# Performance work log

Hardware: AMD Instinct MI355X
Metric: run time of the kernel (lower is better)

The kernel has to match this reference:

```python
import jax, jax.numpy as jnp
import numpy as np

B, Q, K, D = 32, 1024, 1024, 128

def setup_inputs() -> dict:
    key = jax.random.key(0)
    kq, kk, kv, kl = jax.random.split(key, 4)
    return {
        "queries": jax.random.normal(kq, (B, Q, D), dtype=jnp.float32),
        "keys": jax.random.normal(kk, (B, K, D), dtype=jnp.float32),
        "values": jax.random.normal(kv, (B, K, D), dtype=jnp.float32),
        "valid_length": jax.random.randint(kl, (B,), 1, K + 1),
    }

def reference(queries, keys, values, valid_length):
    d = queries.shape[-1]
    # scores: [B, Q, K]
    scores = jnp.einsum("bqd,bkd->bqk", queries, keys) / jnp.sqrt(jnp.float32(d))
    # length mask: position k is valid iff k < valid_length[b]
    mask = jnp.arange(keys.shape[1])[None, None, :] < valid_length[:, None, None]
    scores = jnp.where(mask, scores, jnp.float32(-1e9))
    attn = jax.nn.softmax(scores, axis=-1)
    # dropout module is identity in eval / p=0
    return jnp.einsum("bqk,bkv->bqv", attn, values)
```

## Files before the change

### kernel.cpp

```cpp
#include <hip/hip_runtime.h>
#include <hip/hip_bf16.h>
#include <stdint.h>

#define B_    32
#define QLEN  1024
#define KSEQ  1024
#define DIM   128
#define NKT   (KSEQ / 64)
#define SCALE 0.08838834764831845f
#define KSC   0.12751879522655792f

typedef __attribute__((ext_vector_type(8)))  short short8;
typedef __attribute__((ext_vector_type(4)))  float floatx4;
typedef __attribute__((ext_vector_type(16))) float floatx16;
typedef unsigned int u32;

__device__ __forceinline__ u32 f2bf(float x) {
  union { float f; u32 u; } v; v.f = x;
  return (v.u + 0x7FFF + ((v.u >> 16) & 1)) >> 16;
}
__device__ __forceinline__ u32 pack2(float lo, float hi) {
  return f2bf(lo) | (f2bf(hi) << 16);
}
__device__ __forceinline__ u32 cvtpk(float lo, float hi) {
  u32 d;
  asm("v_cvt_pk_bf16_f32 %0, %1, %2" : "=v"(d) : "v"(lo), "v"(hi));
  return d;
}
__device__ __forceinline__ void swap32(u32& a, u32& b) {
  asm volatile("v_permlane32_swap_b32 %0, %1" : "+v"(a), "+v"(b));
}
__device__ __forceinline__ float exp2_fast(float x) {
  float d;
  asm("v_exp_f32 %0, %1" : "=v"(d) : "v"(x));
  return d;
}
typedef union { uint4 u; short8 s; } U8;

__global__ __launch_bounds__(256) void prep_kernel(const float* __restrict__ Kg,
                                                   const float* __restrict__ Vg,
                                                   const int* __restrict__ vlen,
                                                   uint4* __restrict__ Ksw,
                                                   uint4* __restrict__ Vsw,
                                                   int2* __restrict__ task) {
  __shared__ __align__(16) u32 Vu[64 * 65];
  __shared__ int sidx[32];
  const int kt = blockIdx.x, b = blockIdx.y, t = threadIdx.x;
  const bool tableblk = (blockIdx.z == 0) && (kt == 0) && (b == 0);

  if (tableblk && t < 64) {
    const int bb = t & 31;
    const int ntb = (vlen[bb] + 63) >> 6;
    int rank = 0;
#pragma unroll
    for (int j = 0; j < 32; j++) {
      const int ntj = __shfl(ntb, j);
      rank += (ntj > ntb) | ((ntj == ntb) & (j < bb));
    }
    if (t < 32) sidx[rank] = bb;
  }

  if (kt * 64 < vlen[b]) {
    if (blockIdx.z == 0) {
      const float* src = Kg + ((size_t)b * KSEQ + kt * 64) * DIM;
      uint4* dst = Ksw + ((size_t)b * NKT + kt) * 1024;
#pragma unroll
      for (int it = 0; it < 4; it++) {
        const int f = it * 256 + t, r = f >> 4, c = f & 15;
        floatx4 f0 = *(const floatx4*)(src + r * DIM + c * 8);
        floatx4 f1 = *(const floatx4*)(src + r * DIM + c * 8 + 4);
        uint4 o;
        o.x = pack2(f0[0] * KSC, f0[1] * KSC); o.y = pack2(f0[2] * KSC, f0[3] * KSC);
        o.z = pack2(f1[0] * KSC, f1[1] * KSC); o.w = pack2(f1[2] * KSC, f1[3] * KSC);
        dst[r * 16 + (c ^ (r & 15))] = o;
      }
    } else {
      const float* src = Vg + ((size_t)b * KSEQ + kt * 64) * DIM;
#pragma unroll
      for (int it = 0; it < 8; it++) {
        const int k = it * 8 + (t >> 5), c = t & 31;
        const floatx4 f = *(const floatx4*)(src + (size_t)k * DIM + c * 4);
        const int s = (k >> 3) & 4;
        Vu[k * 65 + ((2 * c) ^ s)]     = pack2(f[0], f[1]);
        Vu[k * 65 + ((2 * c + 1) ^ s)] = pack2(f[2], f[3]);
      }
      __syncthreads();
      uint4* dst = Vsw + ((size_t)b * NKT + kt) * 1024;
#pragma unroll
      for (int it = 0; it < 4; it++) {
        const int id = it * 256 + t;
        const int kc = id & 7, d = (id >> 3) & 127;
        const int col = (d >> 1) ^ (kc & 4);
        u32 r[8];
#pragma unroll
        for (int j = 0; j < 8; j++) r[j] = Vu[(kc * 8 + j) * 65 + col];
        const u32 sel = (d & 1) ? 0x07060302u : 0x05040100u;
        uint4 o;
        o.x = __builtin_amdgcn_perm(r[1], r[0], sel);
        o.y = __builtin_amdgcn_perm(r[3], r[2], sel);
        o.z = __builtin_amdgcn_perm(r[5], r[4], sel);
        o.w = __builtin_amdgcn_perm(r[7], r[6], sel);
        dst[d * 8 + (kc ^ (d & 7))] = o;
      }
    }
  }

  if (tableblk) {
    __syncthreads();
    for (int l = t; l < 512; l += 256) {
      const int x = l & 7, j = l >> 3;
      int rank, q;
      if (j < 32) { rank = (j & 1) ? x + 8  : x;      q = j >> 1; }
      else        { rank = (j & 1) ? x + 16 : x + 24; q = (j - 32) >> 1; }
      task[l] = make_int2(sidx[rank], q << 6);
    }
  }
}

__global__ __launch_bounds__(256, 2) void attn_kernel(
    const float* __restrict__ Qg, const uint4* __restrict__ Ksw,
    const uint4* __restrict__ Vsw, const int* __restrict__ vlen,
    const int2* __restrict__ task, float* __restrict__ Og) {
  __shared__ float scr[64 * 128];
  __shared__ float Lred[2][32];

  const int2 tq = task[blockIdx.x];
  const int b = tq.x, q0 = tq.y;
  const int t = threadIdx.x, wave = t >> 6, lane = t & 63;
  const int qh = wave & 1, kh = wave >> 1;
  const int l31 = lane & 31, hi = lane >> 5, m15 = l31 & 15, m7 = l31 & 7;
  const int L  = vlen[b];
  const int nt = (L + 63) >> 6;
  const int krow = kh * 32 + l31;

  const short* KtS = (const short*)(Ksw + (size_t)b * NKT * 1024);
  const short* Vt  = (const short*)(Vsw + (size_t)b * NKT * 1024);

  short8 qb[8];
  {
    const float* qrow = Qg + ((size_t)b * QLEN + q0 + qh * 32 + l31) * DIM;
#pragma unroll
    for (int c = 0; c < 8; c++) {
      floatx4 f0 = *(const floatx4*)(qrow + c * 16 + hi * 8);
      floatx4 f1 = *(const floatx4*)(qrow + c * 16 + hi * 8 + 4);
      short8 a;
      a[0] = (short)f2bf(f0[0]); a[1] = (short)f2bf(f0[1]);
      a[2] = (short)f2bf(f0[2]); a[3] = (short)f2bf(f0[3]);
      a[4] = (short)f2bf(f1[0]); a[5] = (short)f2bf(f1[1]);
      a[6] = (short)f2bf(f1[2]); a[7] = (short)f2bf(f1[3]);
      qb[c] = a;
    }
  }

  float lrow = 0.0f;
  floatx16 oacc[4];
#pragma unroll
  for (int dt = 0; dt < 4; dt++)
#pragma unroll
    for (int i = 0; i < 16; i++) oacc[dt][i] = 0.0f;

#define LOAD_K(DST, tkv)                                                       \
  {                                                                            \
    const short* kp_ = KtS + (size_t)(tkv) * 8192 + krow * 128;                \
    _Pragma("unroll") for (int c_ = 0; c_ < 8; c_++)                           \
      DST[c_] = *(const short8*)(kp_ + ((2 * c_ + hi) ^ m15) * 8);             \
  }

#define BODY(KF, tkv)                                                          \
  {                                                                            \
    const int k0_ = (tkv) * 64;                                                \
    short8 vb[4][2];                                                           \
    {                                                                          \
      const short* vt_ = Vt + (size_t)(tkv) * 8192;                            \
      _Pragma("unroll") for (int dt = 0; dt < 4; dt++) {                       \
        const short* vr_ = vt_ + (dt * 32 + l31) * 64;                         \
        vb[dt][0] = *(const short8*)(vr_ + ((kh * 4 + 0 + hi) ^ m7) * 8);      \
        vb[dt][1] = *(const short8*)(vr_ + ((kh * 4 + 2 + hi) ^ m7) * 8);      \
      }                                                                        \
    }                                                                          \
    floatx16 s;                                                                \
    _Pragma("unroll") for (int i = 0; i < 16; i++) s[i] = 0.0f;                \
    __builtin_amdgcn_s_setprio(1);                                             \
    _Pragma("unroll") for (int c = 0; c < 8; c++)                              \
      s = __builtin_amdgcn_mfma_f32_32x32x16_bf16(KF[c], qb[c], s, 0, 0, 0);   \
    __builtin_amdgcn_s_setprio(0);                                             \
    if (k0_ + kh * 32 + 32 <= L) {                                             \
      _Pragma("unroll") for (int r = 0; r < 16; r++) {                         \
        s[r] = exp2_fast(s[r]);                                                \
        lrow += s[r];                                                          \
      }                                                                        \
    } else {                                                                   \
      _Pragma("unroll") for (int r = 0; r < 16; r++) {                         \
        const int ck = (r & 3) + 8 * (r >> 2) + 4 * hi;                        \
        const float a = (k0_ + kh * 32 + ck < L) ? exp2_fast(s[r]) : 0.0f;     \
        s[r] = a;                                                              \
        lrow += a;                                                             \
      }                                                                        \
    }                                                                          \
    {                                                                          \
      u32 u0 = cvtpk(s[0], s[1]),   u1 = cvtpk(s[2], s[3]);                    \
      u32 u2 = cvtpk(s[4], s[5]),   u3 = cvtpk(s[6], s[7]);                    \
      swap32(u0, u2); swap32(u1, u3);                                          \
      u32 w0 = cvtpk(s[8], s[9]),   w1 = cvtpk(s[10], s[11]);                  \
      u32 w2 = cvtpk(s[12], s[13]), w3 = cvtpk(s[14], s[15]);                  \
      swap32(w0, w2); swap32(w1, w3);                                          \
      U8 pu0; pu0.u.x = u0; pu0.u.y = u1; pu0.u.z = u2; pu0.u.w = u3;          \
      U8 pu1; pu1.u.x = w0; pu1.u.y = w1; pu1.u.z = w2; pu1.u.w = w3;          \
      __builtin_amdgcn_s_setprio(1);                                           \
      _Pragma("unroll") for (int dt = 0; dt < 4; dt++) {                       \
        oacc[dt] = __builtin_amdgcn_mfma_f32_32x32x16_bf16(pu0.s, vb[dt][0],   \
                                                           oacc[dt], 0, 0, 0);\
        oacc[dt] = __builtin_amdgcn_mfma_f32_32x32x16_bf16(pu1.s, vb[dt][1],   \
                                                           oacc[dt], 0, 0, 0);\
      }                                                                        \
      __builtin_amdgcn_s_setprio(0);                                           \
    }                                                                          \
  }

  short8 ka[8], kb[8];
  LOAD_K(ka, 0);
  int tk = 0;
  for (;;) {
    if (tk + 1 < nt) LOAD_K(kb, tk + 1);
    BODY(ka, tk);
    if (++tk == nt) break;
    if (tk + 1 < nt) LOAD_K(ka, tk + 1);
    BODY(kb, tk);
    if (++tk == nt) break;
  }

  lrow += __shfl_xor(lrow, 32);
  if (kh == 1) {
    if (lane < 32) Lred[qh][l31] = lrow;
#pragma unroll
    for (int dt = 0; dt < 4; dt++)
#pragma unroll
      for (int r = 0; r < 16; r++)
        scr[(dt * 16 + r) * 128 + qh * 64 + lane] = oacc[dt][r];
  }
  __syncthreads();
  if (kh == 0) {
    const float ltot = lrow + Lred[qh][l31];
    const float inv_ = 1.0f / ltot;
    float iv[16];
#pragma unroll
    for (int r = 0; r < 16; r++)
      iv[r] = __shfl(inv_, (r & 3) + 8 * (r >> 2) + 4 * hi);
    float* obase = Og + ((size_t)b * QLEN + q0 + qh * 32) * DIM + l31;
#pragma unroll
    for (int dt = 0; dt < 4; dt++) {
#pragma unroll
      for (int r = 0; r < 16; r++) {
        const int rq = (r & 3) + 8 * (r >> 2) + 4 * hi;
        const float v = oacc[dt][r] + scr[(dt * 16 + r) * 128 + qh * 64 + lane];
        obase[(size_t)rq * DIM + dt * 32] = v * iv[r];
      }
    }
  }
#undef LOAD_K
#undef BODY
}

extern "C" void kernel_launch(void* const* d_in, const int* in_sizes, int n_in,
                              void* d_out, int out_size, void* d_ws, size_t ws_size,
                              hipStream_t stream) {
  const float* Qg = (const float*)d_in[0];
  const float* Kg = (const float*)d_in[1];
  const float* Vg = (const float*)d_in[2];
  const int*  vln = (const int*)d_in[3];
  uint4* Ksw = (uint4*)d_ws;
  uint4* Vsw = (uint4*)((char*)d_ws + (size_t)B_ * NKT * 16384);
  int2*  Tsk = (int2*)((char*)d_ws + 2 * (size_t)B_ * NKT * 16384);

  prep_kernel<<<dim3(NKT, B_, 2), 256, 0, stream>>>(Kg, Vg, vln, Ksw, Vsw, Tsk);
  attn_kernel<<<dim3(512), 256, 0, stream>>>(Qg, Ksw, Vsw, vln, Tsk,
                                             (float*)d_out);
}
```

Baseline: 117.4 us.

## Pre-arrange K and V tiles in per-lane fragment order for coalesced loads

The prep kernel now writes K and V bf16 tiles in exactly the order each attention wave's lanes consume them, so every 16-byte fragment load in the attention kernel is a contiguous per-lane access at a fixed stride. This drops the XOR-swizzled addressing and gives fully coalesced global/L2 reads in the hot loop. K conversion now stages through shared memory with an extra barrier in the prep kernel, which adds some prep cost.

```diff
diff --git a/kernel.cpp b/kernel.cpp
--- a/kernel.cpp
+++ b/kernel.cpp
@@ -44,6 +44,7 @@
                                                    uint4* __restrict__ Vsw,
                                                    int2* __restrict__ task) {
   __shared__ __align__(16) u32 Vu[64 * 65];
+  __shared__ __align__(16) uint4 Ku[64 * 17];
   __shared__ int sidx[32];
   const int kt = blockIdx.x, b = blockIdx.y, t = threadIdx.x;
   const bool tableblk = (blockIdx.z == 0) && (kt == 0) && (b == 0);
@@ -63,7 +64,6 @@
   if (kt * 64 < vlen[b]) {
     if (blockIdx.z == 0) {
       const float* src = Kg + ((size_t)b * KSEQ + kt * 64) * DIM;
-      uint4* dst = Ksw + ((size_t)b * NKT + kt) * 1024;
 #pragma unroll
       for (int it = 0; it < 4; it++) {
         const int f = it * 256 + t, r = f >> 4, c = f & 15;
@@ -72,7 +72,17 @@
         uint4 o;
         o.x = pack2(f0[0] * KSC, f0[1] * KSC); o.y = pack2(f0[2] * KSC, f0[3] * KSC);
         o.z = pack2(f1[0] * KSC, f1[1] * KSC); o.w = pack2(f1[2] * KSC, f1[3] * KSC);
-        dst[r * 16 + (c ^ (r & 15))] = o;
+        Ku[r * 17 + c] = o;
+      }
+      __syncthreads();
+      uint4* dst = Ksw + ((size_t)b * NKT + kt) * 1024;
+#pragma unroll
+      for (int it = 0; it < 4; it++) {
+        const int o16 = it * 256 + t;
+        const int kh = o16 >> 9, cs = (o16 >> 6) & 7, lane = o16 & 63;
+        const int hi = lane >> 5, l31 = lane & 31;
+        const int r = kh * 32 + l31, j = 2 * cs + hi;
+        dst[o16] = Ku[r * 17 + j];
       }
     } else {
       const float* src = Vg + ((size_t)b * KSEQ + kt * 64) * DIM;
@@ -88,8 +98,12 @@
       uint4* dst = Vsw + ((size_t)b * NKT + kt) * 1024;
 #pragma unroll
       for (int it = 0; it < 4; it++) {
-        const int id = it * 256 + t;
-        const int kc = id & 7, d = (id >> 3) & 127;
+        const int o16 = it * 256 + t;
+        const int kh = o16 >> 9, slot = (o16 >> 6) & 7, lane = o16 & 63;
+        const int dt = slot >> 1, i_ = slot & 1;
+        const int hi = lane >> 5, l31 = lane & 31;
+        const int d = dt * 32 + l31, m7 = d & 7;
+        const int kc = (kh * 4 + 2 * i_ + hi);
         const int col = (d >> 1) ^ (kc & 4);
         u32 r[8];
 #pragma unroll
@@ -100,7 +114,7 @@
         o.y = __builtin_amdgcn_perm(r[3], r[2], sel);
         o.z = __builtin_amdgcn_perm(r[5], r[4], sel);
         o.w = __builtin_amdgcn_perm(r[7], r[6], sel);
-        dst[d * 8 + (kc ^ (d & 7))] = o;
+        dst[o16] = o;
       }
     }
   }
@@ -128,13 +142,14 @@
   const int b = tq.x, q0 = tq.y;
   const int t = threadIdx.x, wave = t >> 6, lane = t & 63;
   const int qh = wave & 1, kh = wave >> 1;
-  const int l31 = lane & 31, hi = lane >> 5, m15 = l31 & 15, m7 = l31 & 7;
+  const int l31 = lane & 31, hi = lane >> 5;
   const int L  = vlen[b];
   const int nt = (L + 63) >> 6;
-  const int krow = kh * 32 + l31;
-
-  const short* KtS = (const short*)(Ksw + (size_t)b * NKT * 1024);
-  const short* Vt  = (const short*)(Vsw + (size_t)b * NKT * 1024);
+
+  const short* KtS = (const short*)(Ksw + (size_t)b * NKT * 1024) +
+                     kh * 4096 + lane * 8;
+  const short* Vt  = (const short*)(Vsw + (size_t)b * NKT * 1024) +
+                     kh * 4096 + lane * 8;
 
   short8 qb[8];
   {
@@ -161,9 +176,9 @@
 
 #define LOAD_K(DST, tkv)                                                       \
   {                                                                            \
-    const short* kp_ = KtS + (size_t)(tkv) * 8192 + krow * 128;                \
+    const short* kp_ = KtS + (size_t)(tkv) * 8192;                             \
     _Pragma("unroll") for (int c_ = 0; c_ < 8; c_++)                           \
-      DST[c_] = *(const short8*)(kp_ + ((2 * c_ + hi) ^ m15) * 8);             \
+      DST[c_] = *(const short8*)(kp_ + c_ * 512);                              \
   }
 
 #define BODY(KF, tkv)                                                          \
@@ -173,9 +188,8 @@
     {                                                                          \
       const short* vt_ = Vt + (size_t)(tkv) * 8192;                            \
       _Pragma("unroll") for (int dt = 0; dt < 4; dt++) {                       \
-        const short* vr_ = vt_ + (dt * 32 + l31) * 64;                         \
-        vb[dt][0] = *(const short8*)(vr_ + ((kh * 4 + 0 + hi) ^ m7) * 8);      \
-        vb[dt][1] = *(const short8*)(vr_ + ((kh * 4 + 2 + hi) ^ m7) * 8);      \
+        vb[dt][0] = *(const short8*)(vt_ + (dt * 2 + 0) * 512);                \
+        vb[dt][1] = *(const short8*)(vt_ + (dt * 2 + 1) * 512);                \
       }                                                                        \
     }                                                                          \
     floatx16 s;                                                                \
```

New measurement: 110.8 us. 5.6% less time.
